# Performance work log

Measured on AMD Instinct MI355X. Metric: run time of the kernel, lower is better.

Reference implementation:

```python
import jax, jax.numpy as jnp
import numpy as np

B, S, L = 128, 8192, 32


def setup_inputs() -> dict:
    key = jax.random.key(0)
    k1, k2, k3, k4, k5 = jax.random.split(key, 5)
    logits = jax.random.normal(k1, (B, S, L), dtype=jnp.float32)
    labels = jax.random.randint(k2, (B, S), 0, L)
    loss_mask = jnp.ones((B, S), dtype=bool)
    transitions = jax.random.normal(k3, (L, L), dtype=jnp.float32) * 0.1
    start_transition = jax.random.normal(k4, (L,), dtype=jnp.float32) * 0.1
    end_transition = jax.random.normal(k5, (L,), dtype=jnp.float32) * 0.1
    return {"logits": logits, "labels": labels, "loss_mask": loss_mask,
            "transitions": transitions, "start_transition": start_transition,
            "end_transition": end_transition}


def _denominator(logits, mask, transitions, start_transition, end_transition):
    # forward algorithm in log-space; carry: (B, L) alpha scores
    init = start_transition + logits[:, 0]

    def step(score, xs):
        logits_t, mask_t = xs  # (B, L), (B,)
        # (B, prev L, next L) -> logsumexp over prev
        score_t = jax.nn.logsumexp(
            score[:, :, None] + transitions[None] + logits_t[:, None, :], axis=1)
        score = jnp.where(mask_t[:, None], score_t, score)
        return score, None

    xs = (jnp.swapaxes(logits[:, 1:], 0, 1), jnp.swapaxes(mask[:, 1:], 0, 1))
    final, _ = jax.lax.scan(step, init, xs)
    return jax.nn.logsumexp(final + end_transition, axis=1)  # (B,)


def _numerator(logits, labels, mask, transitions, start_transition, end_transition):
    maskf = mask.astype(logits.dtype)
    arange_b = jnp.arange(logits.shape[0])
    # emission scores for t in [0, S-2], gathered at gold labels
    emis = jnp.take_along_axis(logits[:, :-1], labels[:, :-1, None], axis=2)[..., 0]
    trans_sc = transitions[labels[:, :-1], labels[:, 1:]]  # (B, S-1)
    score = start_transition[labels[:, 0]] + jnp.sum(
        emis * maskf[:, :-1] + trans_sc * maskf[:, 1:], axis=1)
    last_idx = mask.sum(axis=1).astype(jnp.int32) - 1
    last_labels = labels[arange_b, last_idx]
    score = score + logits[arange_b, -1, last_labels] * maskf[:, -1] \
            + end_transition[last_labels]
    return score  # (B,)


def reference(logits, labels, loss_mask, transitions, start_transition, end_transition):
    log_num = _numerator(logits, labels, loss_mask, transitions,
                         start_transition, end_transition)
    log_den = _denominator(logits, loss_mask, transitions,
                           start_transition, end_transition)
    llh = log_num - log_den
    return -jnp.mean(llh)  # reduction='mean'
```

## Files before the change

kernel.cpp:

```cpp
#include <hip/hip_runtime.h>
#include <hip/hip_bf16.h>


typedef float    f32x16 __attribute__((ext_vector_type(16)));
typedef float    f32x2  __attribute__((ext_vector_type(2)));
typedef __bf16   bf16x8 __attribute__((ext_vector_type(8)));
typedef unsigned uint4v __attribute__((ext_vector_type(4)));
typedef unsigned u32x2  __attribute__((ext_vector_type(2)));

#if __has_builtin(__builtin_amdgcn_permlane32_swap)
#define HAVE_PLSWAP 1
#else
#define HAVE_PLSWAP 0
#endif

#define CRF_S 8192
#define CRF_B 128
#define CRF_G 8

__device__ inline unsigned pk_hi16(float a, float b) {
    return __builtin_amdgcn_perm(__builtin_bit_cast(unsigned, b),
                                 __builtin_bit_cast(unsigned, a), 0x07060302u);
}

__device__ inline float fast_exp_m4(float x) {
#if __has_builtin(__builtin_amdgcn_exp2f)
    return __builtin_amdgcn_exp2f(__builtin_fmaf(x, 1.44269504f, -5.77078016f));
#else
    return __expf(x - 4.0f);
#endif
}

__device__ inline f32x16 mfma_pair(bf16x8 Alo, bf16x8 Blo,
                                   bf16x8 Ahi, bf16x8 Bhi) {
    f32x16 z;
    asm("s_nop 1\n\t"
        "v_mfma_f32_32x32x16_bf16 %0, %1, %2, 0\n\t"
        "v_mfma_f32_32x32x16_bf16 %0, %3, %4, %0\n\t"
        "s_nop 7\n\t"
        "s_nop 7\n\t"
        "s_nop 2"
        : "=&v"(z)
        : "v"(Alo), "v"(Blo), "v"(Ahi), "v"(Bhi));
    return z;
}

__device__ inline void crf_renorm(f32x16& acc, float& off) {
    float mx = fmaxf(acc[0], acc[1]);
#pragma unroll
    for (int r = 2; r < 16; ++r) mx = fmaxf(mx, acc[r]);
#pragma unroll
    for (int d = 1; d < 64; d <<= 1) mx = fmaxf(mx, __shfl_xor(mx, d, 64));
    int bits = __builtin_bit_cast(int, mx);
    int e = ((bits >> 23) & 255) - 127;
    if (e < -100) e = 0;
    if (e > 120) e = 120;
    float scale = __builtin_bit_cast(float, (127 - e) << 23);
    acc *= scale;
    off += (float)e * 0.6931471805599453f;
}

__device__ inline void repack_B(const f32x16& acc, int h, bf16x8& Blo, bf16x8& Bhi) {
    unsigned p[8];
#pragma unroll
    for (int i = 0; i < 8; ++i) p[i] = pk_hi16(acc[2 * i], acc[2 * i + 1]);
#if HAVE_PLSWAP
    u32x2 r0 = __builtin_amdgcn_permlane32_swap(p[0], p[2], false, false);
    u32x2 r1 = __builtin_amdgcn_permlane32_swap(p[1], p[3], false, false);
    u32x2 r2 = __builtin_amdgcn_permlane32_swap(p[4], p[6], false, false);
    u32x2 r3 = __builtin_amdgcn_permlane32_swap(p[5], p[7], false, false);
    uint4v bl = {r0[0], r1[0], r0[1], r1[1]};
    uint4v bh = {r2[0], r3[0], r2[1], r3[1]};
#else
    unsigned q[8];
#pragma unroll
    for (int i = 0; i < 8; ++i) q[i] = (unsigned)__shfl_xor((int)p[i], 32, 64);
    bool hiw = (h != 0);
    uint4v bl = { hiw ? q[2] : p[0], hiw ? q[3] : p[1],
                  hiw ? p[2] : q[0], hiw ? p[3] : q[1] };
    uint4v bh = { hiw ? q[6] : p[4], hiw ? q[7] : p[5],
                  hiw ? p[6] : q[4], hiw ? p[7] : q[5] };
#endif
    Blo = __builtin_bit_cast(bf16x8, bl);
    Bhi = __builtin_bit_cast(bf16x8, bh);
}

__global__ __launch_bounds__(256, 1) void crf_phase1(
    const float* __restrict__ logits, const float* __restrict__ trans,
    unsigned* __restrict__ mat16, float* __restrict__ ws_off, int C) {
    const int S = CRF_S;
    int lane = threadIdx.x & 63;
    int wid = blockIdx.x * 4 + (threadIdx.x >> 6);
    int b = wid / C, c = wid - b * C;
    int Lc = S / C;
    int t_lo = c * Lc; if (t_lo == 0) t_lo = 1;
    int t_hi = (c + 1) * Lc;
    int j = lane & 31, h = lane >> 5;
    const float BIAS = 1.001953125f;

    f32x2 e2[8];
#pragma unroll
    for (int i = 0; i < 4; ++i) {
        e2[i][0]     = __expf(trans[(8 * h + 2 * i) * 32 + j]) * BIAS;
        e2[i][1]     = __expf(trans[(8 * h + 2 * i + 1) * 32 + j]) * BIAS;
        e2[4 + i][0] = __expf(trans[(16 + 8 * h + 2 * i) * 32 + j]) * BIAS;
        e2[4 + i][1] = __expf(trans[(16 + 8 * h + 2 * i + 1) * 32 + j]) * BIAS;
    }

    f32x16 acc = {};
#pragma unroll
    for (int r = 0; r < 16; ++r) {
        int row = (r & 3) + 8 * (r >> 2) + 4 * h;
        acc[r] = (row == j) ? 1.0f : 0.0f;
    }

    float off = 0.0f;
    const float* p = logits + (size_t)b * S * 32 + (size_t)t_lo * 32;
    float v_cur = p[j];

    int nsteps = t_hi - t_lo;
    for (int s = 0; s < nsteps - 1; ++s) {
        p += 32;
        float v_nxt = p[j];

        float ev = fast_exp_m4(v_cur);
        f32x2 ev2 = {ev, ev};
        unsigned av[8];
#pragma unroll
        for (int i = 0; i < 8; ++i) {
            f32x2 m = e2[i] * ev2;
            av[i] = pk_hi16(m[0], m[1]);
        }
        bf16x8 Alo = __builtin_bit_cast(bf16x8, (uint4v){av[0], av[1], av[2], av[3]});
        bf16x8 Ahi = __builtin_bit_cast(bf16x8, (uint4v){av[4], av[5], av[6], av[7]});

        bf16x8 Blo, Bhi;
        repack_B(acc, h, Blo, Bhi);
        acc = mfma_pair(Alo, Blo, Ahi, Bhi);

        v_cur = v_nxt;
        if ((s & 15) == 15) crf_renorm(acc, off);
    }
    {
        float ev = fast_exp_m4(v_cur);
        f32x2 ev2 = {ev, ev};
        unsigned av[8];
#pragma unroll
        for (int i = 0; i < 8; ++i) {
            f32x2 m = e2[i] * ev2;
            av[i] = pk_hi16(m[0], m[1]);
        }
        bf16x8 Alo = __builtin_bit_cast(bf16x8, (uint4v){av[0], av[1], av[2], av[3]});
        bf16x8 Ahi = __builtin_bit_cast(bf16x8, (uint4v){av[4], av[5], av[6], av[7]});
        bf16x8 Blo, Bhi;
        repack_B(acc, h, Blo, Bhi);
        acc = mfma_pair(Alo, Blo, Ahi, Bhi);
    }
    crf_renorm(acc, off);
    off += 4.0f * (float)nsteps;

    unsigned* base = mat16 + (size_t)(b * C + c) * 512;
#pragma unroll
    for (int i = 0; i < 8; ++i) {
        int re = ((2 * i) & 3) + 8 * ((2 * i) >> 2) + 4 * h;
        base[j * 16 + (re >> 1)] = pk_hi16(acc[2 * i], acc[2 * i + 1]);
    }
    if (lane == 0) ws_off[b * C + c] = off;
}

__global__ __launch_bounds__(256) void crf_numer(
    const float* __restrict__ logits, const int* __restrict__ labels,
    const float* __restrict__ trans, float* __restrict__ ws_num) {
    const int S = CRF_S;
    int b = blockIdx.x >> 2, seg = blockIdx.x & 3;
    __shared__ float st[1024];
    __shared__ float sred[4];
    for (int i = threadIdx.x; i < 1024; i += 256) st[i] = trans[i];
    __syncthreads();

    const int* lb = labels + (size_t)b * S;
    const float* lg = logits + (size_t)b * S * 32;
    float acc = 0.0f;
    int t0 = seg * (S / 4), t1 = t0 + S / 4;
    for (int t = t0 + threadIdx.x; t < t1; t += 256) {
        int l = lb[t];
        acc += lg[(size_t)t * 32 + l];
        if (t + 1 < S) acc += st[(l << 5) | lb[t + 1]];
    }
#pragma unroll
    for (int d = 1; d < 64; d <<= 1) acc += __shfl_xor(acc, d, 64);
    int wv = threadIdx.x >> 6, lane = threadIdx.x & 63;
    if (lane == 0) sred[wv] = acc;
    __syncthreads();
    if (threadIdx.x == 0)
        atomicAdd(&ws_num[b], sred[0] + sred[1] + sred[2] + sred[3]);
}

__global__ __launch_bounds__(256, 1) void crf_phase2a(
    const unsigned* __restrict__ mat16, const float* __restrict__ ws_off,
    float* __restrict__ gmat, float* __restrict__ goff, int C) {
    int lane = threadIdx.x & 63;
    int wid = blockIdx.x * 4 + (threadIdx.x >> 6);
    int b = wid >> 3, g = wid & 7;
    int j = lane & 31, h = lane >> 5;
    int cpg = C / CRF_G;

    f32x16 acc = {};
#pragma unroll
    for (int r = 0; r < 16; ++r) {
        int row = (r & 3) + 8 * (r >> 2) + 4 * h;
        acc[r] = (row == j) ? 1.0f : 0.0f;
    }
    float off = 0.0f;
    int cbase = b * C + g * cpg;

    for (int s = cpg - 1; s >= 0; --s) {
        const uint4v* Ap = (const uint4v*)(mat16 + (size_t)(cbase + s) * 512);
        bf16x8 Alo = __builtin_bit_cast(bf16x8, Ap[j * 4 + h]);
        bf16x8 Ahi = __builtin_bit_cast(bf16x8, Ap[j * 4 + 2 + h]);
        bf16x8 Blo, Bhi;
        repack_B(acc, h, Blo, Bhi);
        acc = mfma_pair(Alo, Blo, Ahi, Bhi);
        off += ws_off[cbase + s];
    }
    crf_renorm(acc, off);
    float* base = gmat + (size_t)(b * CRF_G + g) * 1024;
#pragma unroll
    for (int r = 0; r < 16; ++r) {
        int row = (r & 3) + 8 * (r >> 2) + 4 * h;
        base[j * 32 + row] = acc[r];
    }
    if (lane == 0) goff[b * CRF_G + g] = off;
}

__global__ __launch_bounds__(64) void crf_phase2b(
    const float* __restrict__ logits, const int* __restrict__ labels,
    const float* __restrict__ startT, const float* __restrict__ endT,
    const float* __restrict__ gmat, const float* __restrict__ goff,
    const float* __restrict__ ws_num, float* __restrict__ out) {
    const int S = CRF_S, G = CRF_G;
    int b = blockIdx.x;
    int lane = threadIdx.x & 63;
    int j = lane & 31;
    __shared__ __align__(16) float sp[2][32];

    float logit0 = logits[(size_t)b * S * 32 + j];
    float sv = startT[j], evv = endT[j];
    float vlog = sv + logit0;
    float m = vlog;
#pragma unroll
    for (int d = 1; d < 32; d <<= 1) m = fmaxf(m, __shfl_xor(m, d, 64));
    float p = __expf(vlog - m);
    float accl = m;

    int buf = 0;
    if (lane < 32) sp[0][j] = p;
    __syncthreads();

    const float* mat = gmat + (size_t)b * G * 1024 + j * 32;
    float4 mreg[8];
#pragma unroll
    for (int i = 0; i < 8; ++i) mreg[i] = ((const float4*)mat)[i];

    for (int c = 0; c < G; ++c) {
        const float* nmat = mat + (size_t)((c + 1 < G) ? c + 1 : c) * 1024;
        float4 nreg[8];
#pragma unroll
        for (int i = 0; i < 8; ++i) nreg[i] = ((const float4*)nmat)[i];

        const float4* spv = (const float4*)sp[buf];
        float vnew = 0.0f;
#pragma unroll
        for (int i = 0; i < 8; ++i) {
            float4 pv = spv[i];
            vnew += pv.x * mreg[i].x + pv.y * mreg[i].y +
                    pv.z * mreg[i].z + pv.w * mreg[i].w;
        }
        float mx = vnew;
#pragma unroll
        for (int d = 1; d < 32; d <<= 1) mx = fmaxf(mx, __shfl_xor(mx, d, 64));
        int bits = __builtin_bit_cast(int, mx);
        int e = ((bits >> 23) & 255) - 127;
        if (e < -100) e = 0;
        if (e > 120) e = 120;
        float scale = __builtin_bit_cast(float, (127 - e) << 23);
        p = vnew * scale;
        accl += (float)e * 0.6931471805599453f + goff[b * G + c];

        buf ^= 1;
        if (lane < 32) sp[buf][j] = p;
        __syncthreads();
#pragma unroll
        for (int i = 0; i < 8; ++i) mreg[i] = nreg[i];
    }

    float tj = p * __expf(evv);
    float ssum = tj;
#pragma unroll
    for (int d = 1; d < 32; d <<= 1) ssum += __shfl_xor(ssum, d, 64);
    float den = accl + __logf(ssum);

    int lab0 = labels[(size_t)b * S];
    int labL = labels[(size_t)b * S + S - 1];
    float num = ws_num[b] + __shfl(sv, lab0, 64) + __shfl(evv, labL, 64);
    if (lane == 0) atomicAdd(out, -(num - den) * (1.0f / (float)CRF_B));
}

extern "C" void kernel_launch(void* const* d_in, const int* in_sizes, int n_in,
                              void* d_out, int out_size, void* d_ws, size_t ws_size,
                              hipStream_t stream) {
    const float* logits = (const float*)d_in[0];
    const int*   labels = (const int*)d_in[1];
    const float* trans  = (const float*)d_in[3];
    const float* startT = (const float*)d_in[4];
    const float* endT   = (const float*)d_in[5];
    float* out = (float*)d_out;

    const int B = CRF_B;
    int C = 64;
    while (C > CRF_G) {
        size_t need = (size_t)B * C * 2048
                    + (size_t)B * CRF_G * 4096
                    + (size_t)B * C * 4 + (size_t)B * CRF_G * 4 + (size_t)B * 4;
        if (need <= ws_size) break;
        C >>= 1;
    }
    unsigned* mat16 = (unsigned*)d_ws;
    float* gmat   = (float*)((char*)d_ws + (size_t)B * C * 2048);
    float* ws_off = gmat + (size_t)B * CRF_G * 1024;
    float* goff   = ws_off + (size_t)B * C;
    float* ws_num = goff + B * CRF_G;

    hipMemsetAsync(out, 0, sizeof(float), stream);
    hipMemsetAsync(ws_num, 0, B * sizeof(float), stream);

    crf_phase1<<<dim3(B * C / 4), dim3(256), 0, stream>>>(
        logits, trans, mat16, ws_off, C);
    crf_phase2a<<<dim3(B * CRF_G / 4), dim3(256), 0, stream>>>(
        mat16, ws_off, gmat, goff, C);
    crf_numer<<<dim3(B * 4), dim3(256), 0, stream>>>(
        logits, labels, trans, ws_num);
    crf_phase2b<<<dim3(B), dim3(64), 0, stream>>>(
        logits, labels, startT, endT, gmat, goff, ws_num, out);
}
```

Baseline: 328.0 us.

## Fuse numerator into phase1 and interleave two chunk chains per wave

```diff
diff --git a/kernel.cpp b/kernel.cpp
--- a/kernel.cpp
+++ b/kernel.cpp
@@ -16,6 +16,7 @@
 
 #define CRF_S 8192
 #define CRF_B 128
+#define CRF_C 64
 #define CRF_G 8
 
 __device__ inline unsigned pk_hi16(float a, float b) {
@@ -85,17 +86,37 @@
     Bhi = __builtin_bit_cast(bf16x8, bh);
 }
 
-__global__ __launch_bounds__(256, 1) void crf_phase1(
-    const float* __restrict__ logits, const float* __restrict__ trans,
-    unsigned* __restrict__ mat16, float* __restrict__ ws_off, int C) {
-    const int S = CRF_S;
-    int lane = threadIdx.x & 63;
+__device__ inline void crf_step(f32x16& acc, float v, int lane, int h,
+                                const f32x2* e2, int labC, int& labP,
+                                const float* __restrict__ trans,
+                                float& emis, float& tr) {
+    tr += trans[labP * 32 + labC];
+    labP = labC;
+    emis += (lane == labC) ? v : 0.0f;
+    float ev = fast_exp_m4(v);
+    f32x2 ev2 = {ev, ev};
+    unsigned av[8];
+#pragma unroll
+    for (int i = 0; i < 8; ++i) {
+        f32x2 m = e2[i] * ev2;
+        av[i] = pk_hi16(m[0], m[1]);
+    }
+    bf16x8 Alo = __builtin_bit_cast(bf16x8, (uint4v){av[0], av[1], av[2], av[3]});
+    bf16x8 Ahi = __builtin_bit_cast(bf16x8, (uint4v){av[4], av[5], av[6], av[7]});
+    bf16x8 Blo, Bhi;
+    repack_B(acc, h, Blo, Bhi);
+    acc = mfma_pair(Alo, Blo, Ahi, Bhi);
+}
+
+__global__ __launch_bounds__(256) void crf_phase1(
+    const float* __restrict__ logits, const int* __restrict__ labels,
+    const float* __restrict__ trans, unsigned* __restrict__ mat16,
+    float* __restrict__ ws_off, float* __restrict__ ws_num2) {
+    const int S = CRF_S, Lc = 128, C = CRF_C;
+    int lane = threadIdx.x & 63, j = lane & 31, h = lane >> 5;
     int wid = blockIdx.x * 4 + (threadIdx.x >> 6);
-    int b = wid / C, c = wid - b * C;
-    int Lc = S / C;
-    int t_lo = c * Lc; if (t_lo == 0) t_lo = 1;
-    int t_hi = (c + 1) * Lc;
-    int j = lane & 31, h = lane >> 5;
+    int b = wid >> 5, k = wid & 31;
+    int cA = k, cB = k + 32;
     const float BIAS = 1.001953125f;
 
     f32x2 e2[8];
@@ -107,103 +128,81 @@
         e2[4 + i][1] = __expf(trans[(16 + 8 * h + 2 * i + 1) * 32 + j]) * BIAS;
     }
 
-    f32x16 acc = {};
+    f32x16 accA = {}, accB = {};
 #pragma unroll
     for (int r = 0; r < 16; ++r) {
         int row = (r & 3) + 8 * (r >> 2) + 4 * h;
-        acc[r] = (row == j) ? 1.0f : 0.0f;
-    }
-
-    float off = 0.0f;
-    const float* p = logits + (size_t)b * S * 32 + (size_t)t_lo * 32;
-    float v_cur = p[j];
-
-    int nsteps = t_hi - t_lo;
-    for (int s = 0; s < nsteps - 1; ++s) {
-        p += 32;
-        float v_nxt = p[j];
-
-        float ev = fast_exp_m4(v_cur);
-        f32x2 ev2 = {ev, ev};
-        unsigned av[8];
-#pragma unroll
-        for (int i = 0; i < 8; ++i) {
-            f32x2 m = e2[i] * ev2;
-            av[i] = pk_hi16(m[0], m[1]);
+        float idv = (row == j) ? 1.0f : 0.0f;
+        accA[r] = idv; accB[r] = idv;
+    }
+
+    int startA = (cA == 0) ? 1 : 0;
+    int nA = Lc - startA, nB = Lc;
+    int tA0 = cA * Lc + startA, tB0 = cB * Lc;
+    const float* pA = logits + ((size_t)b * S + (size_t)tA0) * 32;
+    const float* pB = logits + ((size_t)b * S + (size_t)tB0) * 32;
+    const int* lab = labels + (size_t)b * S;
+    int labPA = lab[tA0 - 1], labPB = lab[tB0 - 1];
+
+    float a0 = pA[j], a1 = pA[32 + j], a2 = pA[64 + j];
+    float b0 = pB[j], b1 = pB[32 + j], b2 = pB[64 + j];
+
+    float emis = 0.0f, tr = 0.0f;
+
+    for (int s = 0; s < 127; ++s) {
+        {
+            int lc = lab[tA0 + s];
+            crf_step(accA, a0, lane, h, e2, lc, labPA, trans, emis, tr);
+            a0 = a1; a1 = a2;
+            int ix = s + 3; if (ix > nA - 1) ix = nA - 1;
+            a2 = pA[(size_t)ix * 32 + j];
         }
-        bf16x8 Alo = __builtin_bit_cast(bf16x8, (uint4v){av[0], av[1], av[2], av[3]});
-        bf16x8 Ahi = __builtin_bit_cast(bf16x8, (uint4v){av[4], av[5], av[6], av[7]});
-
-        bf16x8 Blo, Bhi;
-        repack_B(acc, h, Blo, Bhi);
-        acc = mfma_pair(Alo, Blo, Ahi, Bhi);
-
-        v_cur = v_nxt;
-        if ((s & 15) == 15) crf_renorm(acc, off);
+        {
+            int lc = lab[tB0 + s];
+            crf_step(accB, b0, lane, h, e2, lc, labPB, trans, emis, tr);
+            b0 = b1; b1 = b2;
+            int ix = s + 3; if (ix > nB - 1) ix = nB - 1;
+            b2 = pB[(size_t)ix * 32 + j];
+        }
+    }
+    if (nA == 128) {
+        int lc = lab[tA0 + 127];
+        crf_step(accA, a0, lane, h, e2, lc, labPA, trans, emis, tr);
     }
     {
-        float ev = fast_exp_m4(v_cur);
-        f32x2 ev2 = {ev, ev};
-        unsigned av[8];
-#pragma unroll
-        for (int i = 0; i < 8; ++i) {
-            f32x2 m = e2[i] * ev2;
-            av[i] = pk_hi16(m[0], m[1]);
-        }
-        bf16x8 Alo = __builtin_bit_cast(bf16x8, (uint4v){av[0], av[1], av[2], av[3]});
-        bf16x8 Ahi = __builtin_bit_cast(bf16x8, (uint4v){av[4], av[5], av[6], av[7]});
-        bf16x8 Blo, Bhi;
-        repack_B(acc, h, Blo, Bhi);
-        acc = mfma_pair(Alo, Blo, Ahi, Bhi);
-    }
-    crf_renorm(acc, off);
-    off += 4.0f * (float)nsteps;
-
-    unsigned* base = mat16 + (size_t)(b * C + c) * 512;
+        int lc = lab[tB0 + 127];
+        crf_step(accB, b0, lane, h, e2, lc, labPB, trans, emis, tr);
+    }
+
+    float offA = 0.0f, offB = 0.0f;
+    crf_renorm(accA, offA); offA += 4.0f * (float)nA;
+    crf_renorm(accB, offB); offB += 4.0f * (float)nB;
+
+    unsigned* baseA = mat16 + (size_t)(b * C + cA) * 512;
+    unsigned* baseB = mat16 + (size_t)(b * C + cB) * 512;
 #pragma unroll
     for (int i = 0; i < 8; ++i) {
         int re = ((2 * i) & 3) + 8 * ((2 * i) >> 2) + 4 * h;
-        base[j * 16 + (re >> 1)] = pk_hi16(acc[2 * i], acc[2 * i + 1]);
-    }
-    if (lane == 0) ws_off[b * C + c] = off;
-}
-
-__global__ __launch_bounds__(256) void crf_numer(
-    const float* __restrict__ logits, const int* __restrict__ labels,
-    const float* __restrict__ trans, float* __restrict__ ws_num) {
-    const int S = CRF_S;
-    int b = blockIdx.x >> 2, seg = blockIdx.x & 3;
-    __shared__ float st[1024];
-    __shared__ float sred[4];
-    for (int i = threadIdx.x; i < 1024; i += 256) st[i] = trans[i];
-    __syncthreads();
-
-    const int* lb = labels + (size_t)b * S;
-    const float* lg = logits + (size_t)b * S * 32;
-    float acc = 0.0f;
-    int t0 = seg * (S / 4), t1 = t0 + S / 4;
-    for (int t = t0 + threadIdx.x; t < t1; t += 256) {
-        int l = lb[t];
-        acc += lg[(size_t)t * 32 + l];
-        if (t + 1 < S) acc += st[(l << 5) | lb[t + 1]];
-    }
-#pragma unroll
-    for (int d = 1; d < 64; d <<= 1) acc += __shfl_xor(acc, d, 64);
-    int wv = threadIdx.x >> 6, lane = threadIdx.x & 63;
-    if (lane == 0) sred[wv] = acc;
-    __syncthreads();
-    if (threadIdx.x == 0)
-        atomicAdd(&ws_num[b], sred[0] + sred[1] + sred[2] + sred[3]);
-}
-
-__global__ __launch_bounds__(256, 1) void crf_phase2a(
+        baseA[j * 16 + (re >> 1)] = pk_hi16(accA[2 * i], accA[2 * i + 1]);
+        baseB[j * 16 + (re >> 1)] = pk_hi16(accB[2 * i], accB[2 * i + 1]);
+    }
+#pragma unroll
+    for (int d = 1; d < 64; d <<= 1) emis += __shfl_xor(emis, d, 64);
+    if (lane == 0) {
+        ws_off[b * C + cA] = offA;
+        ws_off[b * C + cB] = offB;
+        ws_num2[b * 32 + k] = emis + tr;
+    }
+}
+
+__global__ __launch_bounds__(256) void crf_phase2a(
     const unsigned* __restrict__ mat16, const float* __restrict__ ws_off,
-    float* __restrict__ gmat, float* __restrict__ goff, int C) {
+    float* __restrict__ gmat, float* __restrict__ goff) {
     int lane = threadIdx.x & 63;
     int wid = blockIdx.x * 4 + (threadIdx.x >> 6);
     int b = wid >> 3, g = wid & 7;
     int j = lane & 31, h = lane >> 5;
-    int cpg = C / CRF_G;
+    int cpg = CRF_C / CRF_G;
 
     f32x16 acc = {};
 #pragma unroll
@@ -212,7 +211,7 @@
         acc[r] = (row == j) ? 1.0f : 0.0f;
     }
     float off = 0.0f;
-    int cbase = b * C + g * cpg;
+    int cbase = b * CRF_C + g * cpg;
 
     for (int s = cpg - 1; s >= 0; --s) {
         const uint4v* Ap = (const uint4v*)(mat16 + (size_t)(cbase + s) * 512);
@@ -237,7 +236,7 @@
     const float* __restrict__ logits, const int* __restrict__ labels,
     const float* __restrict__ startT, const float* __restrict__ endT,
     const float* __restrict__ gmat, const float* __restrict__ goff,
-    const float* __restrict__ ws_num, float* __restrict__ out) {
+    const float* __restrict__ ws_num2, float* __restrict__ out) {
     const int S = CRF_S, G = CRF_G;
     int b = blockIdx.x;
     int lane = threadIdx.x & 63;
@@ -300,9 +299,14 @@
     for (int d = 1; d < 32; d <<= 1) ssum += __shfl_xor(ssum, d, 64);
     float den = accl + __logf(ssum);
 
+    float nsum = (lane < 32) ? ws_num2[b * 32 + lane] : 0.0f;
+#pragma unroll
+    for (int d = 1; d < 64; d <<= 1) nsum += __shfl_xor(nsum, d, 64);
+
     int lab0 = labels[(size_t)b * S];
     int labL = labels[(size_t)b * S + S - 1];
-    float num = ws_num[b] + __shfl(sv, lab0, 64) + __shfl(evv, labL, 64);
+    float num = nsum + __shfl(sv, lab0, 64) + __shfl(logit0, lab0, 64) +
+                __shfl(evv, labL, 64);
     if (lane == 0) atomicAdd(out, -(num - den) * (1.0f / (float)CRF_B));
 }
 
@@ -316,30 +320,19 @@
     const float* endT   = (const float*)d_in[5];
     float* out = (float*)d_out;
 
-    const int B = CRF_B;
-    int C = 64;
-    while (C > CRF_G) {
-        size_t need = (size_t)B * C * 2048
-                    + (size_t)B * CRF_G * 4096
-                    + (size_t)B * C * 4 + (size_t)B * CRF_G * 4 + (size_t)B * 4;
-        if (need <= ws_size) break;
-        C >>= 1;
-    }
+    const int B = CRF_B, C = CRF_C;
     unsigned* mat16 = (unsigned*)d_ws;
     float* gmat   = (float*)((char*)d_ws + (size_t)B * C * 2048);
     float* ws_off = gmat + (size_t)B * CRF_G * 1024;
     float* goff   = ws_off + (size_t)B * C;
-    float* ws_num = goff + B * CRF_G;
+    float* ws_num2 = goff + B * CRF_G;
 
     hipMemsetAsync(out, 0, sizeof(float), stream);
-    hipMemsetAsync(ws_num, 0, B * sizeof(float), stream);
-
-    crf_phase1<<<dim3(B * C / 4), dim3(256), 0, stream>>>(
-        logits, trans, mat16, ws_off, C);
+
+    crf_phase1<<<dim3(B * 32 / 4), dim3(256), 0, stream>>>(
+        logits, labels, trans, mat16, ws_off, ws_num2);
     crf_phase2a<<<dim3(B * CRF_G / 4), dim3(256), 0, stream>>>(
-        mat16, ws_off, gmat, goff, C);
-    crf_numer<<<dim3(B * 4), dim3(256), 0, stream>>>(
-        logits, labels, trans, ws_num);
+        mat16, ws_off, gmat, goff);
     crf_phase2b<<<dim3(B), dim3(64), 0, stream>>>(
-        logits, labels, startT, endT, gmat, goff, ws_num, out);
-}
+        logits, labels, startT, endT, gmat, goff, ws_num2, out);
+}
```

New measurement: 321.4 us. 2.0% less time.
